# Optimization experiments

Measured on AMD Instinct MI355X. Metric: run time of the kernel, lower is better.

## Reference

```python
import jax, jax.numpy as jnp
import numpy as np

B, T, V, D, H, HS, FF, L = 4, 1024, 32000, 1024, 16, 64, 4096, 8
STD = 0.02

def _ln(x, g, b, eps=1e-5):
    m = x.mean(-1, keepdims=True)
    v = ((x - m) ** 2).mean(-1, keepdims=True)
    return (x - m) / jnp.sqrt(v + eps) * g + b

def setup_inputs() -> dict:
    key = jax.random.key(0)
    ks = jax.random.split(key, 16)
    n = lambda k, shp: jax.random.normal(k, shp, dtype=jnp.float32) * STD
    inp = {
        "idx": jax.random.randint(ks[0], (B, T), 0, V),
        "tok_emb": n(ks[1], (V, D)),
        "pos_emb": n(ks[2], (T, D)),
        # per-layer stacked attention weights; [D, H, HS] per layer (no bias)
        "Wq": n(ks[3], (L, D, H, HS)),
        "Wk": n(ks[4], (L, D, H, HS)),
        "Wv": n(ks[5], (L, D, H, HS)),
        "Wp": n(ks[6], (L, H * HS, D)),
        "bp": jnp.zeros((L, D), jnp.float32),
        "ln1_g": jnp.ones((L, D), jnp.float32),
        "ln1_b": jnp.zeros((L, D), jnp.float32),
        "ln2_g": jnp.ones((L, D), jnp.float32),
        "ln2_b": jnp.zeros((L, D), jnp.float32),
        "W1": n(ks[7], (L, D, FF)),
        "b1": jnp.zeros((L, FF), jnp.float32),
        "W2": n(ks[8], (L, FF, D)),
        "b2": jnp.zeros((L, D), jnp.float32),
        "lnf_g": jnp.ones((D,), jnp.float32),
        "lnf_b": jnp.zeros((D,), jnp.float32),
        "Wlm": n(ks[9], (D, V)),
        "blm": jnp.zeros((V,), jnp.float32),
    }
    return inp

def reference(idx, tok_emb, pos_emb, Wq, Wk, Wv, Wp, bp, ln1_g, ln1_b,
              ln2_g, ln2_b, W1, b1, W2, b2, lnf_g, lnf_b, Wlm, blm):
    Bb, Tt = idx.shape
    x = tok_emb[idx] + pos_emb[:Tt]                      # [B,T,D]
    causal = jnp.tril(jnp.ones((Tt, Tt), bool))          # tril mask
    for l in range(L):
        xn = _ln(x, ln1_g[l], ln1_b[l])
        q = jnp.einsum('btd,dhk->bhtk', xn, Wq[l])
        k = jnp.einsum('btd,dhk->bhtk', xn, Wk[l])
        v = jnp.einsum('btd,dhk->bhtk', xn, Wv[l])
        w = jnp.einsum('bhtk,bhsk->bhts', q, k) * (HS ** -0.5)
        w = jnp.where(causal, w, -jnp.inf)
        w = jax.nn.softmax(w, axis=-1)
        o = jnp.einsum('bhts,bhsk->bhtk', w, v)
        o = o.transpose(0, 2, 1, 3).reshape(Bb, Tt, H * HS)  # concat heads
        x = x + o @ Wp[l] + bp[l]
        xn = _ln(x, ln2_g[l], ln2_b[l])
        x = x + jax.nn.relu(xn @ W1[l] + b1[l]) @ W2[l] + b2[l]
    x = _ln(x, lnf_g, lnf_b)
    logits = x @ Wlm + blm                               # [B,T,V]
    return logits
```

## Files before the change

kernel.cpp:

```cpp
#include <hip/hip_runtime.h>
#include <cstdint>

typedef __attribute__((ext_vector_type(4))) float f32x4;
typedef __attribute__((ext_vector_type(8))) short s16x8;
typedef unsigned short u16;
typedef unsigned int u32;
typedef __attribute__((address_space(1))) void gas_void;
typedef __attribute__((address_space(3))) void las_void;

#define B_ 4
#define T_ 1024
#define V_ 32000
#define D_ 1024
#define H_ 16
#define HS_ 64
#define FF_ 4096
#define L_ 8
#define BT_ (B_ * T_)

__device__ __forceinline__ float bf2f(u16 h) { return __uint_as_float(((u32)h) << 16); }
__device__ __forceinline__ u16 f2bf(float f) {
  u32 u = __float_as_uint(f);
  u += 0x7fffu + ((u >> 16) & 1u);
  return (u16)(u >> 16);
}

__device__ __forceinline__ void gld16(const void* g, void* l) {
  __builtin_amdgcn_global_load_lds((gas_void*)(uintptr_t)g,
                                   (las_void*)(u32)(uintptr_t)l, 16, 0, 0);
}


template <int EPI>
__global__ __launch_bounds__(512, 2) void gemm256(
    const u16* __restrict__ A, const u16* __restrict__ Bt,
    const float* __restrict__ bias, float* Cf, u16* Cb,
    int M, int N, int K, int nrowb) {
  __shared__ u16 lds[2][2][2][8192];
  const int tid = threadIdx.x;
  const int lane = tid & 63;
  const int lr = lane & 15, hi = lane >> 4;
  const int wid = tid >> 6;
  const int wm128 = (wid >> 2) << 7;
  const int wn64 = (wid & 3) << 6;
  const int logical = ((int)blockIdx.x & 7) * ((int)gridDim.x >> 3) + ((int)blockIdx.x >> 3);
  const int row0 = (logical % nrowb) << 8;
  const int col0 = (logical / nrowb) << 8;
  const int NT = K >> 6;
  const int srow = tid >> 2;
  const int schunk = tid & 3;
  const int xo = ((hi + (lr >> 1)) & 3) << 4;

  f32x4 acc[32];
#pragma unroll
  for (int i = 0; i < 32; ++i) acc[i] = f32x4{0.f, 0.f, 0.f, 0.f};
  s16x8 bfr[4];

#define VMW(N) asm volatile("s_waitcnt vmcnt(" #N ")" ::: "memory")

#define STG(DB, DK, OP, KT)                                                    \
  {                                                                            \
    const u16* sp_ = (OP) ? Bt : A;                                            \
    const int base_ = (OP) ? col0 : row0;                                      \
    const int c0_ = ((KT) << 6) + ((DK) << 5);                                 \
    _Pragma("unroll")                                                          \
    for (int sh_ = 0; sh_ < 2; ++sh_) {                                        \
      const int rr_ = (sh_ << 7) + srow;                                       \
      const int ko_ = ((schunk - (rr_ >> 1)) & 3) << 3;                        \
      gld16(sp_ + (size_t)(base_ + rr_) * K + c0_ + ko_,                       \
            (char*)&lds[DB][DK][OP][0] + (sh_ << 13) + (wid << 10));           \
    }                                                                          \
  }

#define PHASE(BUF, MH, KS, LOADB, STG_STMT, VM_STMT)                           \
  {                                                                            \
    __builtin_amdgcn_sched_barrier(0);                                         \
    const char* As_ = (const char*)&lds[BUF][KS][0][0];                        \
    const char* Bs_ = (const char*)&lds[BUF][KS][1][0];                        \
    const int ra_ = wm128 + ((MH) << 6) + lr;                                  \
    s16x8 af_[4];                                                              \
    _Pragma("unroll")                                                          \
    for (int q_ = 0; q_ < 4; ++q_)                                             \
      af_[q_] = *(const s16x8*)(As_ + ((ra_ + (q_ << 4)) << 6) + xo);          \
    if (LOADB) {                                                               \
      _Pragma("unroll")                                                        \
      for (int q_ = 0; q_ < 4; ++q_)                                           \
        bfr[q_] = *(const s16x8*)(Bs_ + ((wn64 + lr + (q_ << 4)) << 6) + xo);  \
    }                                                                          \
    STG_STMT;                                                                  \
    __builtin_amdgcn_sched_barrier(0);                                         \
    __builtin_amdgcn_s_barrier();                                              \
    asm volatile("s_waitcnt lgkmcnt(0)" ::: "memory");                         \
    __builtin_amdgcn_sched_barrier(0);                                         \
    __builtin_amdgcn_s_setprio(1);                                             \
    _Pragma("unroll")                                                          \
    for (int mi_ = 0; mi_ < 4; ++mi_) {                                        \
      _Pragma("unroll")                                                        \
      for (int nj_ = 0; nj_ < 4; ++nj_)                                        \
        acc[((MH)*4 + mi_) * 4 + nj_] = __builtin_amdgcn_mfma_f32_16x16x32_bf16( \
            af_[mi_], bfr[nj_], acc[((MH)*4 + mi_) * 4 + nj_], 0, 0, 0);       \
    }                                                                          \
    __builtin_amdgcn_s_setprio(0);                                             \
    __builtin_amdgcn_sched_barrier(0);                                         \
    VM_STMT;                                                                   \
    __builtin_amdgcn_s_barrier();                                              \
  }

  STG(0, 0, 0, 0)
  STG(0, 0, 1, 0)
  STG(0, 1, 0, 0)
  STG(0, 1, 1, 0)
  STG(1, 0, 0, 1)
  STG(1, 0, 1, 1)
  VMW(8);
  __builtin_amdgcn_s_barrier();

  const int NI = NT >> 1;
  for (int it = 0; it < NI - 1; ++it) {
    const int t1 = 2 * it + 1, t2 = 2 * it + 2, t3 = 2 * it + 3;
    PHASE(0, 0, 0, 1, STG(1, 1, 0, t1), )
    PHASE(0, 1, 0, 0, STG(1, 1, 1, t1), VMW(6))
    PHASE(0, 0, 1, 1, STG(0, 0, 0, t2), )
    PHASE(0, 1, 1, 0, STG(0, 0, 1, t2), VMW(6))
    PHASE(1, 0, 0, 1, STG(0, 1, 0, t2), )
    PHASE(1, 1, 0, 0, STG(0, 1, 1, t2), VMW(6))
    PHASE(1, 0, 1, 1, STG(1, 0, 0, t3), )
    PHASE(1, 1, 1, 0, STG(1, 0, 1, t3), VMW(6))
  }
  {
    PHASE(0, 0, 0, 1, STG(1, 1, 0, NT - 1), )
    PHASE(0, 1, 0, 0, STG(1, 1, 1, NT - 1), VMW(8))
    PHASE(0, 0, 1, 1, (void)0, )
    PHASE(0, 1, 1, 0, (void)0, VMW(4))
    PHASE(1, 0, 0, 1, (void)0, )
    PHASE(1, 1, 0, 0, (void)0, VMW(0))
    PHASE(1, 0, 1, 1, (void)0, )
    PHASE(1, 1, 1, 0, (void)0, )
  }
#undef PHASE
#undef STG
#undef VMW

  const int gr0 = row0 + wm128;
  const int gc0 = col0 + wn64;
#pragma unroll
  for (int nj = 0; nj < 4; ++nj) {
    const int col = gc0 + (nj << 4) + lr;
    const float bv = (EPI != 0) ? bias[col] : 0.f;
#pragma unroll
    for (int mi = 0; mi < 8; ++mi) {
#pragma unroll
      for (int rg = 0; rg < 4; ++rg) {
        const int row = gr0 + (mi << 4) + (hi << 2) + rg;
        const size_t off = (size_t)row * N + col;
        float val = acc[mi * 4 + nj][rg] + bv;
        if constexpr (EPI == 2) val = fmaxf(val, 0.f);
        if constexpr (EPI == 0 || EPI == 2) Cb[off] = f2bf(val);
        else Cf[off] = val;
      }
    }
  }
}

template <int EPI>
__global__ __launch_bounds__(256) void gemm_bt(
    const u16* __restrict__ A, const u16* __restrict__ Bt,
    const float* __restrict__ bias, float* Cf, u16* Cb,
    int M, int N, int K) {
  __shared__ u16 lds[2][2][4096];
  const int tid = threadIdx.x;
  const int lane = tid & 63;
  const int lr = lane & 15, hi = lane >> 4;
  const int wid = tid >> 6;
  const int wm = wid >> 1, wn = wid & 1;
  const int row0 = blockIdx.y << 7, col0 = blockIdx.x << 7;
  const int NT = K >> 5;
  const int wbase = (tid & ~63) << 4;
  const int xo = ((hi + (lr >> 1)) & 3) << 4;

  f32x4 acc[4][4];
#pragma unroll
  for (int i = 0; i < 4; ++i)
#pragma unroll
    for (int j = 0; j < 4; ++j) acc[i][j] = f32x4{0.f, 0.f, 0.f, 0.f};

  auto stage = [&](int buf, int kt) {
#pragma unroll
    for (int c = 0; c < 2; ++c) {
      const int o = (c << 12) + (tid << 4);
      const int r = o >> 6;
      const int ko = ((((o >> 4) & 3) - (r >> 1)) & 3) << 3;
      gld16(A + (size_t)(row0 + r) * K + (kt << 5) + ko,
            (char*)&lds[buf][0][0] + (c << 12) + wbase);
      gld16(Bt + (size_t)(col0 + r) * K + (kt << 5) + ko,
            (char*)&lds[buf][1][0] + (c << 12) + wbase);
    }
  };

  stage(0, 0);
  __syncthreads();
  int cur = 0;
  for (int kt = 0; kt < NT; ++kt) {
    if (kt + 1 < NT) stage(cur ^ 1, kt + 1);
    const char* As = (const char*)&lds[cur][0][0];
    const char* Bs = (const char*)&lds[cur][1][0];
    s16x8 af[4], bfr[4];
#pragma unroll
    for (int i = 0; i < 4; ++i) {
      const int ra = (wm << 6) + (i << 4) + lr;
      af[i] = *(const s16x8*)(As + (ra << 6) + xo);
      const int rb = (wn << 6) + (i << 4) + lr;
      bfr[i] = *(const s16x8*)(Bs + (rb << 6) + xo);
    }
#pragma unroll
    for (int i = 0; i < 4; ++i)
#pragma unroll
      for (int j = 0; j < 4; ++j)
        acc[i][j] =
            __builtin_amdgcn_mfma_f32_16x16x32_bf16(af[i], bfr[j], acc[i][j], 0, 0, 0);
    __syncthreads();
    cur ^= 1;
  }

  const int gr = row0 + (wm << 6);
  const int gc = col0 + (wn << 6);
#pragma unroll
  for (int j = 0; j < 4; ++j) {
    const int col = gc + (j << 4) + lr;
    const float bv = (EPI != 0) ? bias[col] : 0.f;
#pragma unroll
    for (int i = 0; i < 4; ++i) {
#pragma unroll
      for (int rg = 0; rg < 4; ++rg) {
        const int row = gr + (i << 4) + (hi << 2) + rg;
        const size_t off = (size_t)row * N + col;
        float val = acc[i][j][rg] + bv;
        if constexpr (EPI == 1) val += Cf[off];
        if constexpr (EPI == 2) val = fmaxf(val, 0.f);
        if constexpr (EPI == 0 || EPI == 2) Cb[off] = f2bf(val);
        else Cf[off] = val;
      }
    }
  }
}

__global__ __launch_bounds__(256) void ln_kernel(const float* __restrict__ x,
                                                 const float* __restrict__ gw,
                                                 const float* __restrict__ bw,
                                                 u16* __restrict__ out) {
  const int r = blockIdx.x, tid = threadIdx.x;
  const int lane = tid & 63, wid = tid >> 6;
  __shared__ float red[8];
  f32x4 v = *(const f32x4*)(x + ((size_t)r << 10) + (tid << 2));
  float s = v[0] + v[1] + v[2] + v[3];
  float q = v[0] * v[0] + v[1] * v[1] + v[2] * v[2] + v[3] * v[3];
#pragma unroll
  for (int off = 32; off; off >>= 1) {
    s += __shfl_down(s, off);
    q += __shfl_down(q, off);
  }
  if (lane == 0) {
    red[wid] = s;
    red[4 + wid] = q;
  }
  __syncthreads();
  const float mean = (red[0] + red[1] + red[2] + red[3]) * (1.f / 1024.f);
  const float var = (red[4] + red[5] + red[6] + red[7]) * (1.f / 1024.f) - mean * mean;
  const float rstd = rsqrtf(var + 1e-5f);
  f32x4 g4 = *(const f32x4*)(gw + (tid << 2));
  f32x4 b4 = *(const f32x4*)(bw + (tid << 2));
  u16* op = out + ((size_t)r << 10) + (tid << 2);
#pragma unroll
  for (int j = 0; j < 4; ++j) op[j] = f2bf((v[j] - mean) * rstd * g4[j] + b4[j]);
}

__global__ __launch_bounds__(256) void embed_kernel(const int* __restrict__ idx,
                                                    const float* __restrict__ tok,
                                                    const float* __restrict__ pos,
                                                    float* __restrict__ x) {
  const int r = blockIdx.x, tid = threadIdx.x;
  const int t = r & (T_ - 1);
  const int tk = idx[r];
  f32x4 a = *(const f32x4*)(tok + ((size_t)tk << 10) + (tid << 2));
  f32x4 p = *(const f32x4*)(pos + ((size_t)t << 10) + (tid << 2));
  *(f32x4*)(x + ((size_t)r << 10) + (tid << 2)) = a + p;
}

__global__ __launch_bounds__(256) void tconv_kernel(const float* __restrict__ src,
                                                    u16* __restrict__ dst, int K, int N) {
  __shared__ float tile[32][33];
  const int tx = threadIdx.x & 31, ty = threadIdx.x >> 5;
  const int n0 = blockIdx.x << 5, k0 = blockIdx.y << 5;
#pragma unroll
  for (int i = 0; i < 32; i += 8)
    tile[ty + i][tx] = src[(size_t)(k0 + ty + i) * N + n0 + tx];
  __syncthreads();
#pragma unroll
  for (int i = 0; i < 32; i += 8)
    dst[(size_t)(n0 + ty + i) * K + k0 + tx] = f2bf(tile[tx][ty + i]);
}

__global__ __launch_bounds__(256) void fattn_kernel(const u16* __restrict__ qkv,
                                                    u16* __restrict__ o) {
  const int qt = blockIdx.x, h = blockIdx.y, b = blockIdx.z;
  const int tid = threadIdx.x;
  const int lane = tid & 63;
  const int lr = lane & 15, hi = lane >> 4;
  const int w = tid >> 6;
  __shared__ u16 Kl[4096];
  __shared__ u16 Vt[4096];
  __shared__ u16 Pl[4][1024];

  const int q_row = (qt << 6) + (w << 4) + lr;
  const size_t qbase = ((size_t)(b * T_) + q_row) * 3072 + (h << 6);
  s16x8 aq[2];
  aq[0] = *(const s16x8*)(qkv + qbase + hi * 8);
  aq[1] = *(const s16x8*)(qkv + qbase + 32 + hi * 8);

  f32x4 ofr[4];
  float m[4], lsum[4];
#pragma unroll
  for (int j = 0; j < 4; ++j) ofr[j] = f32x4{0.f, 0.f, 0.f, 0.f};
#pragma unroll
  for (int rg = 0; rg < 4; ++rg) { m[rg] = -1e30f; lsum[rg] = 0.f; }

  const size_t bT = (size_t)(b * T_);

  for (int kt = 0; kt <= qt; ++kt) {
    const int kv0 = kt << 6;
#pragma unroll
    for (int sh = 0; sh < 2; ++sh) {
      const int ob = (sh << 12) + (tid << 4);
      const int r = ob >> 7;
      const int il = (ob & 127) ^ ((r & 7) << 4);
      gld16(qkv + (bT + kv0 + r) * 3072 + 1024 + (h << 6) + (il >> 1),
            (char*)Kl + (sh << 12) + ((tid & 192) << 4));
    }
#pragma unroll
    for (int sh = 0; sh < 2; ++sh) {
      const int c = (w << 1) + sh;
      uint4 pv = *(const uint4*)(qkv + (bT + kv0 + lane) * 3072 + 2048 +
                                 (h << 6) + (c << 3));
#pragma unroll
      for (int j = 0; j < 8; ++j) {
        const int d = (c << 3) + j;
        Vt[(d << 6) + (lane ^ ((d & 7) << 3))] = ((const u16*)&pv)[j];
      }
    }
    __syncthreads();

    f32x4 s[4];
#pragma unroll
    for (int j = 0; j < 4; ++j) s[j] = f32x4{0.f, 0.f, 0.f, 0.f};
#pragma unroll
    for (int kk = 0; kk < 2; ++kk)
#pragma unroll
      for (int j = 0; j < 4; ++j) {
        const int rb = (j << 4) + lr;
        const s16x8 bk = *(const s16x8*)((const char*)Kl + (rb << 7) +
                                         ((((kk << 2) + hi) ^ (rb & 7)) << 4));
        s[j] = __builtin_amdgcn_mfma_f32_16x16x32_bf16(aq[kk], bk, s[j], 0, 0, 0);
      }

    const bool diag = (kt == qt);
#pragma unroll
    for (int j = 0; j < 4; ++j) {
      f32x4 sv = s[j] * 0.125f;
      if (diag) {
        const int col = (j << 4) + lr;
#pragma unroll
        for (int rg = 0; rg < 4; ++rg) {
          const int row = (w << 4) + (hi << 2) + rg;
          if (col > row) sv[rg] = -1e30f;
        }
      }
      s[j] = sv;
    }

#pragma unroll
    for (int rg = 0; rg < 4; ++rg) {
      float mx = fmaxf(fmaxf(s[0][rg], s[1][rg]), fmaxf(s[2][rg], s[3][rg]));
      mx = fmaxf(mx, __shfl_xor(mx, 1));
      mx = fmaxf(mx, __shfl_xor(mx, 2));
      mx = fmaxf(mx, __shfl_xor(mx, 4));
      mx = fmaxf(mx, __shfl_xor(mx, 8));
      const float mn = fmaxf(m[rg], mx);
      const float sc = __expf(m[rg] - mn);
      m[rg] = mn;
      float rs = 0.f;
#pragma unroll
      for (int j = 0; j < 4; ++j) {
        const float e = __expf(s[j][rg] - mn);
        s[j][rg] = e;
        rs += e;
      }
      rs += __shfl_xor(rs, 1);
      rs += __shfl_xor(rs, 2);
      rs += __shfl_xor(rs, 4);
      rs += __shfl_xor(rs, 8);
      lsum[rg] = lsum[rg] * sc + rs;
#pragma unroll
      for (int j2 = 0; j2 < 4; ++j2) ofr[j2][rg] *= sc;
    }

#pragma unroll
    for (int j = 0; j < 4; ++j)
#pragma unroll
      for (int rg = 0; rg < 4; ++rg) {
        const int row = (hi << 2) + rg, col = (j << 4) + lr;
        Pl[w][(row << 6) + (col ^ ((row & 7) << 3))] = f2bf(s[j][rg]);
      }

#pragma unroll
    for (int kk = 0; kk < 2; ++kk) {
      const s16x8 ap = *(const s16x8*)((const char*)&Pl[w][0] + (lr << 7) +
                                       (((kk << 6) + (hi << 4)) ^ ((lr & 7) << 4)));
#pragma unroll
      for (int j2 = 0; j2 < 4; ++j2) {
        const int rb = (j2 << 4) + lr;
        const s16x8 bv = *(const s16x8*)((const char*)Vt + (rb << 7) +
                                         ((((kk << 2) + hi) ^ (rb & 7)) << 4));
        ofr[j2] = __builtin_amdgcn_mfma_f32_16x16x32_bf16(ap, bv, ofr[j2], 0, 0, 0);
      }
    }
    __syncthreads();
  }

  float rinv[4];
#pragma unroll
  for (int rg = 0; rg < 4; ++rg) rinv[rg] = 1.f / lsum[rg];
#pragma unroll
  for (int j2 = 0; j2 < 4; ++j2)
#pragma unroll
    for (int rg = 0; rg < 4; ++rg) {
      const int row = (qt << 6) + (w << 4) + (hi << 2) + rg;
      const int col = (h << 6) + (j2 << 4) + lr;
      o[(bT + row) * 1024 + col] = f2bf(ofr[j2][rg] * rinv[rg]);
    }
}

extern "C" void kernel_launch(void* const* d_in, const int* in_sizes, int n_in,
                              void* d_out, int out_size, void* d_ws, size_t ws_size,
                              hipStream_t stream) {
  (void)in_sizes; (void)n_in; (void)out_size; (void)ws_size;
  const int* idx = (const int*)d_in[0];
  const float* tokE = (const float*)d_in[1];
  const float* posE = (const float*)d_in[2];
  const float* Wq = (const float*)d_in[3];
  const float* Wk = (const float*)d_in[4];
  const float* Wv = (const float*)d_in[5];
  const float* Wp = (const float*)d_in[6];
  const float* bp = (const float*)d_in[7];
  const float* ln1g = (const float*)d_in[8];
  const float* ln1b = (const float*)d_in[9];
  const float* ln2g = (const float*)d_in[10];
  const float* ln2b = (const float*)d_in[11];
  const float* W1 = (const float*)d_in[12];
  const float* b1 = (const float*)d_in[13];
  const float* W2 = (const float*)d_in[14];
  const float* b2 = (const float*)d_in[15];
  const float* lnfg = (const float*)d_in[16];
  const float* lnfb = (const float*)d_in[17];
  const float* Wlm = (const float*)d_in[18];
  const float* blm = (const float*)d_in[19];

  char* p = (char*)d_ws;
  float* x = (float*)p;   p += (size_t)BT_ * D_ * 4;
  u16* xn = (u16*)p;      p += (size_t)BT_ * D_ * 2;
  u16* qkv = (u16*)p;     p += (size_t)BT_ * 3072 * 2;
  u16* ob = (u16*)p;      p += (size_t)BT_ * D_ * 2;
  u16* hb = (u16*)p;      p += (size_t)BT_ * FF_ * 2;
  u16* WqkvT = (u16*)p;   p += (size_t)L_ * 3072 * D_ * 2;
  u16* WpT = (u16*)p;     p += (size_t)L_ * D_ * D_ * 2;
  u16* W1T = (u16*)p;     p += (size_t)L_ * FF_ * D_ * 2;
  u16* W2T = (u16*)p;     p += (size_t)L_ * D_ * FF_ * 2;
  u16* WlmT = (u16*)p;    p += (size_t)V_ * D_ * 2;

  dim3 blk(256);
  dim3 blk512(512);
  for (int l = 0; l < L_; ++l) {
    tconv_kernel<<<dim3(32, 32), blk, 0, stream>>>(Wq + (size_t)l * D_ * D_,
                                                   WqkvT + (size_t)l * 3072 * D_, D_, D_);
    tconv_kernel<<<dim3(32, 32), blk, 0, stream>>>(
        Wk + (size_t)l * D_ * D_, WqkvT + (size_t)l * 3072 * D_ + D_ * D_, D_, D_);
    tconv_kernel<<<dim3(32, 32), blk, 0, stream>>>(
        Wv + (size_t)l * D_ * D_, WqkvT + (size_t)l * 3072 * D_ + 2 * D_ * D_, D_, D_);
    tconv_kernel<<<dim3(32, 32), blk, 0, stream>>>(Wp + (size_t)l * D_ * D_,
                                                   WpT + (size_t)l * D_ * D_, D_, D_);
    tconv_kernel<<<dim3(128, 32), blk, 0, stream>>>(W1 + (size_t)l * D_ * FF_,
                                                    W1T + (size_t)l * FF_ * D_, D_, FF_);
    tconv_kernel<<<dim3(32, 128), blk, 0, stream>>>(W2 + (size_t)l * FF_ * D_,
                                                    W2T + (size_t)l * D_ * FF_, FF_, D_);
  }
  tconv_kernel<<<dim3(1000, 32), blk, 0, stream>>>(Wlm, WlmT, D_, V_);

  embed_kernel<<<dim3(BT_), blk, 0, stream>>>(idx, tokE, posE, x);

  for (int l = 0; l < L_; ++l) {
    ln_kernel<<<dim3(BT_), blk, 0, stream>>>(x, ln1g + l * D_, ln1b + l * D_, xn);
    gemm256<0><<<dim3(192), blk512, 0, stream>>>(xn, WqkvT + (size_t)l * 3072 * D_,
                                                 nullptr, nullptr, qkv, BT_, 3072, D_, 16);
    fattn_kernel<<<dim3(T_ / 64, H_, B_), blk, 0, stream>>>(qkv, ob);
    gemm_bt<1><<<dim3(8, 32), blk, 0, stream>>>(ob, WpT + (size_t)l * D_ * D_,
                                                bp + l * D_, x, nullptr, BT_, D_, D_);
    ln_kernel<<<dim3(BT_), blk, 0, stream>>>(x, ln2g + l * D_, ln2b + l * D_, xn);
    gemm256<2><<<dim3(256), blk512, 0, stream>>>(xn, W1T + (size_t)l * FF_ * D_,
                                                 b1 + l * FF_, nullptr, hb, BT_, FF_, D_, 16);
    gemm_bt<1><<<dim3(8, 32), blk, 0, stream>>>(hb, W2T + (size_t)l * D_ * FF_,
                                                b2 + l * D_, x, nullptr, BT_, D_, FF_);
  }
  ln_kernel<<<dim3(BT_), blk, 0, stream>>>(x, lnfg, lnfb, xn);
  gemm256<3><<<dim3(2000), blk512, 0, stream>>>(xn, WlmT, blm, (float*)d_out, nullptr,
                                                BT_, V_, D_, 16);
}
```

Before: 3.048 ms.

## Double-buffer K/V tiles in flash attention and keep P in registers

```diff
diff --git a/kernel.cpp b/kernel.cpp
--- a/kernel.cpp
+++ b/kernel.cpp
@@ -3,6 +3,7 @@
 
 typedef __attribute__((ext_vector_type(4))) float f32x4;
 typedef __attribute__((ext_vector_type(8))) short s16x8;
+typedef __attribute__((ext_vector_type(4))) short s16x4;
 typedef unsigned short u16;
 typedef unsigned int u32;
 typedef __attribute__((address_space(1))) void gas_void;
@@ -307,136 +308,176 @@
   const int lane = tid & 63;
   const int lr = lane & 15, hi = lane >> 4;
   const int w = tid >> 6;
-  __shared__ u16 Kl[4096];
-  __shared__ u16 Vt[4096];
-  __shared__ u16 Pl[4][1024];
-
+  __shared__ alignas(16) u16 Kl[2][4096];
+  __shared__ alignas(16) u16 Vt[2][4096];
+
+  const size_t bT = (size_t)(b * T_);
   const int q_row = (qt << 6) + (w << 4) + lr;
-  const size_t qbase = ((size_t)(b * T_) + q_row) * 3072 + (h << 6);
+  const size_t qbase = (bT + q_row) * 3072 + (h << 6);
   s16x8 aq[2];
   aq[0] = *(const s16x8*)(qkv + qbase + hi * 8);
   aq[1] = *(const s16x8*)(qkv + qbase + 32 + hi * 8);
 
   f32x4 ofr[4];
-  float m[4], lsum[4];
 #pragma unroll
   for (int j = 0; j < 4; ++j) ofr[j] = f32x4{0.f, 0.f, 0.f, 0.f};
-#pragma unroll
-  for (int rg = 0; rg < 4; ++rg) { m[rg] = -1e30f; lsum[rg] = 0.f; }
-
-  const size_t bT = (size_t)(b * T_);
-
+  float mrun = -1e30f, lsum = 0.f;
+
+  uint4 vr0, vr1;
+
+#define STAGEK(BUF, KT)                                                        \
+  {                                                                            \
+    _Pragma("unroll")                                                          \
+    for (int sh_ = 0; sh_ < 2; ++sh_) {                                        \
+      const int ob_ = (sh_ << 12) + (tid << 4);                                \
+      const int r_ = ob_ >> 7;                                                 \
+      const int il_ = (ob_ & 127) ^ ((r_ & 7) << 4);                           \
+      gld16(qkv + (bT + ((KT) << 6) + r_) * 3072 + 1024 + (h << 6) + (il_ >> 1), \
+            (char*)&Kl[BUF][0] + (sh_ << 12) + ((tid & 192) << 4));            \
+    }                                                                          \
+  }
+#define LOADV(KT)                                                              \
+  {                                                                            \
+    const u16* vs_ =                                                           \
+        qkv + (bT + ((KT) << 6) + lane) * 3072 + 2048 + (h << 6) + (w << 4);   \
+    vr0 = *(const uint4*)vs_;                                                  \
+    vr1 = *(const uint4*)(vs_ + 8);                                            \
+  }
+#define WRITEV(BUF)                                                            \
+  {                                                                            \
+    const u16* p0_ = (const u16*)&vr0;                                         \
+    const u16* p1_ = (const u16*)&vr1;                                         \
+    _Pragma("unroll")                                                          \
+    for (int j_ = 0; j_ < 8; ++j_) {                                           \
+      const int sw_ = lane ^ (j_ << 3);                                        \
+      Vt[BUF][(((w << 4) + j_) << 6) + sw_] = p0_[j_];                         \
+      Vt[BUF][(((w << 4) + 8 + j_) << 6) + sw_] = p1_[j_];                     \
+    }                                                                          \
+  }
+
+  STAGEK(0, 0)
+  LOADV(0)
+  asm volatile("s_waitcnt vmcnt(0)" ::: "memory");
+  WRITEV(0)
+  asm volatile("s_waitcnt lgkmcnt(0)" ::: "memory");
+  __builtin_amdgcn_sched_barrier(0);
+  __builtin_amdgcn_s_barrier();
+
+  int cur = 0;
   for (int kt = 0; kt <= qt; ++kt) {
-    const int kv0 = kt << 6;
-#pragma unroll
-    for (int sh = 0; sh < 2; ++sh) {
-      const int ob = (sh << 12) + (tid << 4);
-      const int r = ob >> 7;
-      const int il = (ob & 127) ^ ((r & 7) << 4);
-      gld16(qkv + (bT + kv0 + r) * 3072 + 1024 + (h << 6) + (il >> 1),
-            (char*)Kl + (sh << 12) + ((tid & 192) << 4));
-    }
-#pragma unroll
-    for (int sh = 0; sh < 2; ++sh) {
-      const int c = (w << 1) + sh;
-      uint4 pv = *(const uint4*)(qkv + (bT + kv0 + lane) * 3072 + 2048 +
-                                 (h << 6) + (c << 3));
-#pragma unroll
-      for (int j = 0; j < 8; ++j) {
-        const int d = (c << 3) + j;
-        Vt[(d << 6) + (lane ^ ((d & 7) << 3))] = ((const u16*)&pv)[j];
-      }
-    }
-    __syncthreads();
+    if (kt < qt) {
+      STAGEK(cur ^ 1, kt + 1)
+      LOADV(kt + 1)
+    }
 
     f32x4 s[4];
 #pragma unroll
     for (int j = 0; j < 4; ++j) s[j] = f32x4{0.f, 0.f, 0.f, 0.f};
+    __builtin_amdgcn_s_setprio(1);
 #pragma unroll
     for (int kk = 0; kk < 2; ++kk)
 #pragma unroll
       for (int j = 0; j < 4; ++j) {
         const int rb = (j << 4) + lr;
-        const s16x8 bk = *(const s16x8*)((const char*)Kl + (rb << 7) +
+        const s16x8 bk = *(const s16x8*)((const char*)&Kl[cur][0] + (rb << 7) +
                                          ((((kk << 2) + hi) ^ (rb & 7)) << 4));
-        s[j] = __builtin_amdgcn_mfma_f32_16x16x32_bf16(aq[kk], bk, s[j], 0, 0, 0);
+        s[j] = __builtin_amdgcn_mfma_f32_16x16x32_bf16(bk, aq[kk], s[j], 0, 0, 0);
       }
-
-    const bool diag = (kt == qt);
-#pragma unroll
-    for (int j = 0; j < 4; ++j) {
-      f32x4 sv = s[j] * 0.125f;
-      if (diag) {
-        const int col = (j << 4) + lr;
+    __builtin_amdgcn_s_setprio(0);
+
+    if (kt == qt) {
+      const int qr = (w << 4) + lr;
+#pragma unroll
+      for (int j = 0; j < 4; ++j)
 #pragma unroll
         for (int rg = 0; rg < 4; ++rg) {
-          const int row = (w << 4) + (hi << 2) + rg;
-          if (col > row) sv[rg] = -1e30f;
+          const int kvr = (j << 4) + (hi << 2) + rg;
+          s[j][rg] = (kvr > qr) ? -1e30f : s[j][rg] * 0.125f;
         }
-      }
-      s[j] = sv;
-    }
-
-#pragma unroll
-    for (int rg = 0; rg < 4; ++rg) {
-      float mx = fmaxf(fmaxf(s[0][rg], s[1][rg]), fmaxf(s[2][rg], s[3][rg]));
-      mx = fmaxf(mx, __shfl_xor(mx, 1));
-      mx = fmaxf(mx, __shfl_xor(mx, 2));
-      mx = fmaxf(mx, __shfl_xor(mx, 4));
-      mx = fmaxf(mx, __shfl_xor(mx, 8));
-      const float mn = fmaxf(m[rg], mx);
-      const float sc = __expf(m[rg] - mn);
-      m[rg] = mn;
-      float rs = 0.f;
-#pragma unroll
-      for (int j = 0; j < 4; ++j) {
+    } else {
+#pragma unroll
+      for (int j = 0; j < 4; ++j) s[j] = s[j] * 0.125f;
+    }
+
+    float mx = -1e30f;
+#pragma unroll
+    for (int j = 0; j < 4; ++j)
+#pragma unroll
+      for (int rg = 0; rg < 4; ++rg) mx = fmaxf(mx, s[j][rg]);
+    mx = fmaxf(mx, __shfl_xor(mx, 16));
+    mx = fmaxf(mx, __shfl_xor(mx, 32));
+    const float mn = fmaxf(mrun, mx);
+    const float sc = __expf(mrun - mn);
+    mrun = mn;
+    float rs = 0.f;
+#pragma unroll
+    for (int j = 0; j < 4; ++j)
+#pragma unroll
+      for (int rg = 0; rg < 4; ++rg) {
         const float e = __expf(s[j][rg] - mn);
         s[j][rg] = e;
         rs += e;
       }
-      rs += __shfl_xor(rs, 1);
-      rs += __shfl_xor(rs, 2);
-      rs += __shfl_xor(rs, 4);
-      rs += __shfl_xor(rs, 8);
-      lsum[rg] = lsum[rg] * sc + rs;
-#pragma unroll
-      for (int j2 = 0; j2 < 4; ++j2) ofr[j2][rg] *= sc;
-    }
-
-#pragma unroll
-    for (int j = 0; j < 4; ++j)
-#pragma unroll
-      for (int rg = 0; rg < 4; ++rg) {
-        const int row = (hi << 2) + rg, col = (j << 4) + lr;
-        Pl[w][(row << 6) + (col ^ ((row & 7) << 3))] = f2bf(s[j][rg]);
+    rs += __shfl_xor(rs, 16);
+    rs += __shfl_xor(rs, 32);
+    lsum = lsum * sc + rs;
+    float scO[4];
+#pragma unroll
+    for (int rg = 0; rg < 4; ++rg) scO[rg] = __shfl(sc, (hi << 2) + rg);
+#pragma unroll
+    for (int j2 = 0; j2 < 4; ++j2)
+#pragma unroll
+      for (int rg = 0; rg < 4; ++rg) ofr[j2][rg] *= scO[rg];
+
+    s16x8 pb[2];
+#pragma unroll
+    for (int kk = 0; kk < 2; ++kk)
+#pragma unroll
+      for (int i = 0; i < 4; ++i) {
+        pb[kk][i] = (short)f2bf(s[2 * kk][i]);
+        pb[kk][4 + i] = (short)f2bf(s[2 * kk + 1][i]);
       }
 
-#pragma unroll
-    for (int kk = 0; kk < 2; ++kk) {
-      const s16x8 ap = *(const s16x8*)((const char*)&Pl[w][0] + (lr << 7) +
-                                       (((kk << 6) + (hi << 4)) ^ ((lr & 7) << 4)));
+    __builtin_amdgcn_s_setprio(1);
+#pragma unroll
+    for (int kk = 0; kk < 2; ++kk)
 #pragma unroll
       for (int j2 = 0; j2 < 4; ++j2) {
-        const int rb = (j2 << 4) + lr;
-        const s16x8 bv = *(const s16x8*)((const char*)Vt + (rb << 7) +
-                                         ((((kk << 2) + hi) ^ (rb & 7)) << 4));
-        ofr[j2] = __builtin_amdgcn_mfma_f32_16x16x32_bf16(ap, bv, ofr[j2], 0, 0, 0);
+        const int drow = (j2 << 4) + lr;
+        const int swz = (drow & 7) << 3;
+        const int base = drow << 6;
+        const s16x4 lo = *(const s16x4*)&Vt[cur][base + (((kk << 5) + (hi << 2)) ^ swz)];
+        const s16x4 hv = *(const s16x4*)&Vt[cur][base + (((kk << 5) + 16 + (hi << 2)) ^ swz)];
+        const s16x8 vb = __builtin_shufflevector(lo, hv, 0, 1, 2, 3, 4, 5, 6, 7);
+        ofr[j2] = __builtin_amdgcn_mfma_f32_16x16x32_bf16(pb[kk], vb, ofr[j2], 0, 0, 0);
       }
-    }
-    __syncthreads();
-  }
-
-  float rinv[4];
-#pragma unroll
-  for (int rg = 0; rg < 4; ++rg) rinv[rg] = 1.f / lsum[rg];
+    __builtin_amdgcn_s_setprio(0);
+
+    if (kt < qt) {
+      asm volatile("s_waitcnt vmcnt(0)" ::: "memory");
+      WRITEV(cur ^ 1)
+    }
+    asm volatile("s_waitcnt lgkmcnt(0)" ::: "memory");
+    __builtin_amdgcn_sched_barrier(0);
+    __builtin_amdgcn_s_barrier();
+    cur ^= 1;
+  }
+
+  const float rinv = 1.f / lsum;
+  float rO[4];
+#pragma unroll
+  for (int rg = 0; rg < 4; ++rg) rO[rg] = __shfl(rinv, (hi << 2) + rg);
 #pragma unroll
   for (int j2 = 0; j2 < 4; ++j2)
 #pragma unroll
     for (int rg = 0; rg < 4; ++rg) {
       const int row = (qt << 6) + (w << 4) + (hi << 2) + rg;
       const int col = (h << 6) + (j2 << 4) + lr;
-      o[(bT + row) * 1024 + col] = f2bf(ofr[j2][rg] * rinv[rg]);
-    }
+      o[(bT + row) * 1024 + col] = f2bf(ofr[j2][rg] * rO[rg]);
+    }
+#undef STAGEK
+#undef LOADV
+#undef WRITEV
 }
 
 extern "C" void kernel_launch(void* const* d_in, const int* in_sizes, int n_in,
@@ -498,8 +539,8 @@
 
   for (int l = 0; l < L_; ++l) {
     ln_kernel<<<dim3(BT_), blk, 0, stream>>>(x, ln1g + l * D_, ln1b + l * D_, xn);
-    gemm256<0><<<dim3(192), blk512, 0, stream>>>(xn, WqkvT + (size_t)l * 3072 * D_,
-                                                 nullptr, nullptr, qkv, BT_, 3072, D_, 16);
+    gemm_bt<0><<<dim3(24, 32), blk, 0, stream>>>(xn, WqkvT + (size_t)l * 3072 * D_,
+                                                 nullptr, nullptr, qkv, BT_, 3072, D_);
     fattn_kernel<<<dim3(T_ / 64, H_, B_), blk, 0, stream>>>(qkv, ob);
     gemm_bt<1><<<dim3(8, 32), blk, 0, stream>>>(ob, WpT + (size_t)l * D_ * D_,
                                                 bp + l * D_, x, nullptr, BT_, D_, D_);
```

Result: faster. 2.967 ms (-2.7%).
